# Kernel optimization log

Measured on AMD Instinct MI355X. Metric: run time of the kernel, lower is better.

The kernel has to match this reference:

```python
import jax, jax.numpy as jnp
import numpy as np

SPARSITY = 0.01
NUM_BLOCKS = 8

def _softshrink(v, lam):
    return jnp.sign(v) * jnp.maximum(jnp.abs(v) - lam, 0.0)

def setup_inputs() -> dict:
    key = jax.random.key(0)
    ks = jax.random.split(key, 5)
    B, H, W, C = 4, 128, 128, 768
    nb, bs = NUM_BLOCKS, C // NUM_BLOCKS
    return {
        "x": jax.random.normal(ks[0], (B, H, W, C), dtype=jnp.float32),
        "w1": jax.random.normal(ks[1], (2, nb, bs, bs), dtype=jnp.float32) * 0.02,
        "b1": jax.random.normal(ks[2], (2, nb, bs), dtype=jnp.float32) * 0.02,
        "w2": jax.random.normal(ks[3], (2, nb, bs, bs), dtype=jnp.float32) * 0.02,
        "b2": jax.random.normal(ks[4], (2, nb, bs), dtype=jnp.float32) * 0.02,
    }

def reference(x, w1, b1, w2, b2):
    B, H, W, C = x.shape
    nb = NUM_BLOCKS
    bs = C // nb
    # FFT token mixing (ortho-normalized), real->complex half-spectrum
    xf = jnp.fft.rfft2(x, axes=(1, 2), norm="ortho")  # [B, H, W//2+1, C]
    Hf, Wf = xf.shape[1], xf.shape[2]
    xr = xf.real.reshape(B, Hf, Wf, nb, bs)
    xi = xf.imag.reshape(B, Hf, Wf, nb, bs)
    # kept_modes = H*W//2+1 with hard_thresholding_fraction=1 >= Wf -> all modes kept
    # Block-diagonal complex MLP layer 1 + GELU (exact, matching torch nn.GELU)
    o1r = jax.nn.gelu(
        jnp.einsum("bhwni,nio->bhwno", xr, w1[0])
        - jnp.einsum("bhwni,nio->bhwno", xi, w1[1]) + b1[0],
        approximate=False)
    o1i = jax.nn.gelu(
        jnp.einsum("bhwni,nio->bhwno", xi, w1[0])
        + jnp.einsum("bhwni,nio->bhwno", xr, w1[1]) + b1[1],
        approximate=False)
    # Layer 2 (complex matmul), then softshrink on real/imag parts
    o2r = (jnp.einsum("bhwni,nio->bhwno", o1r, w2[0])
           - jnp.einsum("bhwni,nio->bhwno", o1i, w2[1]) + b2[0])
    o2i = (jnp.einsum("bhwni,nio->bhwno", o1i, w2[0])
           + jnp.einsum("bhwni,nio->bhwno", o1r, w2[1]) + b2[1])
    o2r = _softshrink(o2r, SPARSITY)
    o2i = _softshrink(o2i, SPARSITY)
    xc = (o2r + 1j * o2i).reshape(B, Hf, Wf, C)
    out = jnp.fft.irfft2(xc, s=(H, W), axes=(1, 2), norm="ortho")
    return out
```

## Files before the change

kernel.cpp:

```cpp
#include <hip/hip_runtime.h>
#include <hip/hip_bf16.h>
#include <math.h>

typedef __bf16 bfx8 __attribute__((ext_vector_type(8)));
typedef __bf16 bfx4 __attribute__((ext_vector_type(4)));
typedef float f32x4 __attribute__((ext_vector_type(4)));

__device__ __forceinline__ int bitrev7(int x) {
  return ((x & 1) << 6) | ((x & 2) << 4) | ((x & 4) << 2) | (x & 8)
       | ((x & 16) >> 2) | ((x & 32) >> 4) | ((x & 64) >> 6);
}

__device__ __forceinline__ void bfly(float& ar, float& ai, float& br, float& bi,
                                     float tc, float ts) {
  float dr = ar - br, di = ai - bi;
  ar += br; ai += bi;
  br = dr * tc - di * ts;
  bi = dr * ts + di * tc;
}

__device__ __forceinline__ void build_tw(float2* tw, float sign, int tid) {
  if (tid < 64) {
    float s_, c_;
    __sincosf(sign * (float)(2.0 * M_PI / 128.0) * (float)tid, &s_, &c_);
    tw[tid] = make_float2(c_, s_);
  }
}

__device__ __forceinline__ void fft_stages04(float (&xr)[4][8], float (&xi)[4][8],
                                             const float2* tw, int wq) {
  #pragma unroll
  for (int a = 0; a < 8; ++a) {
    #pragma unroll
    for (int b = 0; b < 2; ++b) {
      float2 t = tw[wq + 4 * a + 32 * b];
      bfly(xr[b][a], xi[b][a], xr[b + 2][a], xi[b + 2][a], t.x, t.y);
    }
  }
  #pragma unroll
  for (int a = 0; a < 8; ++a) {
    float2 t = tw[2 * (wq + 4 * a)];
    bfly(xr[0][a], xi[0][a], xr[1][a], xi[1][a], t.x, t.y);
    bfly(xr[2][a], xi[2][a], xr[3][a], xi[3][a], t.x, t.y);
  }
  #pragma unroll
  for (int a = 0; a < 4; ++a) {
    float2 t = tw[4 * (wq + 4 * a)];
    #pragma unroll
    for (int b = 0; b < 4; ++b)
      bfly(xr[b][a], xi[b][a], xr[b][a + 4], xi[b][a + 4], t.x, t.y);
  }
  {
    float2 t0 = tw[8 * wq];
    float2 t1 = tw[8 * (wq + 4)];
    #pragma unroll
    for (int b = 0; b < 4; ++b) {
      bfly(xr[b][0], xi[b][0], xr[b][2], xi[b][2], t0.x, t0.y);
      bfly(xr[b][1], xi[b][1], xr[b][3], xi[b][3], t1.x, t1.y);
      bfly(xr[b][4], xi[b][4], xr[b][6], xi[b][6], t0.x, t0.y);
      bfly(xr[b][5], xi[b][5], xr[b][7], xi[b][7], t1.x, t1.y);
    }
  }
  {
    float2 t = tw[16 * wq];
    #pragma unroll
    for (int b = 0; b < 4; ++b) {
      #pragma unroll
      for (int a = 0; a < 8; a += 2)
        bfly(xr[b][a], xi[b][a], xr[b][a + 1], xi[b][a + 1], t.x, t.y);
    }
  }
}

__device__ __forceinline__ void fft_stages56(float (&yr)[4], float (&yi)[4], float sign) {
  float dr, di;
  dr = yr[0] - yr[2]; di = yi[0] - yi[2];
  yr[0] += yr[2]; yi[0] += yi[2]; yr[2] = dr; yi[2] = di;
  dr = yr[1] - yr[3]; di = yi[1] - yi[3];
  yr[1] += yr[3]; yi[1] += yi[3];
  yr[3] = -sign * di; yi[3] = sign * dr;
  dr = yr[0] - yr[1]; di = yi[0] - yi[1];
  yr[0] += yr[1]; yi[0] += yi[1]; yr[1] = dr; yi[1] = di;
  dr = yr[2] - yr[3]; di = yi[2] - yi[3];
  yr[2] += yr[3]; yi[2] += yi[3]; yr[3] = dr; yi[3] = di;
}

__global__ __launch_bounds__(256, 2) void k_fftw_fwd(
    const float* __restrict__ x, float* __restrict__ Xr, float* __restrict__ Xi) {
  __shared__ float2 l[128 * 64];
  __shared__ float2 tw[64];
  const int bh = blockIdx.x;
  const int c0 = blockIdx.y * 64;
  const int tid = threadIdx.x;
  const int c = tid & 63, wq = tid >> 6;
  build_tw(tw, -1.f, tid);
  const float* xrow = x + (size_t)bh * (128 * 768) + c0 + c;
  float xr[4][8], xi_[4][8];
  #pragma unroll
  for (int b = 0; b < 4; ++b)
    #pragma unroll
    for (int a = 0; a < 8; ++a) {
      int p = wq + 4 * a + 32 * b;
      xr[b][a] = xrow[(size_t)p * 768];
      xi_[b][a] = 0.f;
    }
  __syncthreads();
  fft_stages04(xr, xi_, tw, wq);
  #pragma unroll
  for (int b = 0; b < 4; ++b)
    #pragma unroll
    for (int a = 0; a < 8; ++a) {
      int p = wq + 4 * a + 32 * b;
      l[p * 64 + c] = make_float2(xr[b][a], xi_[b][a]);
    }
  __syncthreads();
  const float sc = 1.f / 128.f;
  #pragma unroll
  for (int t = 0; t < 8; ++t) {
    int g = wq + 4 * t;
    float yr[4], yi[4];
    #pragma unroll
    for (int d = 0; d < 4; ++d) {
      float2 v = l[(4 * g + d) * 64 + c];
      yr[d] = v.x; yi[d] = v.y;
    }
    fft_stages56(yr, yi, -1.f);
    #pragma unroll
    for (int d = 0; d < 4; ++d) {
      int f = bitrev7(4 * g + d);
      if (f < 65) {
        Xr[((size_t)bh * 65 + f) * 768 + c0 + c]  = yr[d] * sc;
        Xi[((size_t)bh * 128 + f) * 768 + c0 + c] = yi[d] * sc;
      }
    }
  }
}

__global__ __launch_bounds__(256, 2) void k_ffth(
    float* Xr, float* Xi, float sign, float scale) {
  __shared__ float2 l[128 * 64];
  __shared__ float2 tw[64];
  const int bw = blockIdx.x;
  const int b = bw / 65, wf = bw % 65;
  const int c0 = blockIdx.y * 64;
  const int tid = threadIdx.x;
  const int c = tid & 63, wq = tid >> 6;
  build_tw(tw, sign, tid);
  const size_t baser = ((size_t)b * 128 * 65 + wf) * 768 + c0 + c;
  const size_t basei = ((size_t)b * 128 * 128 + wf) * 768 + c0 + c;
  float xr[4][8], xi_[4][8];
  #pragma unroll
  for (int bb = 0; bb < 4; ++bb)
    #pragma unroll
    for (int a = 0; a < 8; ++a) {
      int p = wq + 4 * a + 32 * bb;
      xr[bb][a]  = Xr[baser + (size_t)p * (65 * 768)];
      xi_[bb][a] = Xi[basei + (size_t)p * (128 * 768)];
    }
  __syncthreads();
  fft_stages04(xr, xi_, tw, wq);
  #pragma unroll
  for (int bb = 0; bb < 4; ++bb)
    #pragma unroll
    for (int a = 0; a < 8; ++a) {
      int p = wq + 4 * a + 32 * bb;
      l[p * 64 + c] = make_float2(xr[bb][a], xi_[bb][a]);
    }
  __syncthreads();
  #pragma unroll
  for (int t = 0; t < 8; ++t) {
    int g = wq + 4 * t;
    float yr[4], yi[4];
    #pragma unroll
    for (int d = 0; d < 4; ++d) {
      float2 v = l[(4 * g + d) * 64 + c];
      yr[d] = v.x; yi[d] = v.y;
    }
    fft_stages56(yr, yi, sign);
    #pragma unroll
    for (int d = 0; d < 4; ++d) {
      int hf = bitrev7(4 * g + d);
      Xr[baser + (size_t)hf * (65 * 768)]  = yr[d] * scale;
      Xi[basei + (size_t)hf * (128 * 768)] = yi[d] * scale;
    }
  }
}

__global__ void k_wprep(const float* __restrict__ w1, const float* __restrict__ w2,
                        float* __restrict__ out) {
  int e = blockIdx.x * 256 + threadIdx.x;
  int kin8 = e % 12;
  int t = e / 12;
  int oc = t % 96;
  int t2 = t / 96;
  int n = t2 & 7;
  int q = t2 >> 3;
  int L = q >> 1, ri = q & 1;
  const float* src = (L ? w2 : w1) + (size_t)ri * 73728 + ((size_t)n * 96) * 96 + oc;
  bfx8 v;
  #pragma unroll
  for (int j = 0; j < 8; ++j)
    v[j] = (__bf16)src[(size_t)(kin8 * 8 + j) * 96];
  __bf16* wt = (__bf16*)(out + ((size_t)q * 128 + 65) * 768);
  *(bfx8*)&wt[((size_t)(n * 96 + oc)) * 96 + kin8 * 8] = v;
}

#define MPB 208
__device__ __forceinline__ bfx8 neg8(bfx8 v) {
  union { bfx8 b; unsigned int u[4]; } t;
  t.b = v;
  t.u[0] ^= 0x80008000u; t.u[1] ^= 0x80008000u;
  t.u[2] ^= 0x80008000u; t.u[3] ^= 0x80008000u;
  return t.b;
}

__global__ __launch_bounds__(256, 4) void k_mlp(
    float* __restrict__ Xr, float* __restrict__ Xi,
    const __bf16* __restrict__ wt0,
    const float* __restrict__ b1, const float* __restrict__ b2) {
  __shared__ __align__(16) unsigned char O1[2 * 64 * MPB];

  const int n = blockIdx.y;
  const int m0 = blockIdx.x * 64;
  const int tid = threadIdx.x;
  const int lane = tid & 63;
  const int w = tid >> 6;
  const int col = lane & 15;
  const int quad = lane >> 4;
  const int mrow = w * 16 + col;
  const int m = m0 + mrow;
  const int bh = m / 65, wf = m - bh * 65;
  const size_t xr_base = (size_t)m * 768 + n * 96;
  const size_t xi_base = ((size_t)bh * 128 + wf) * 768 + n * 96;
  const __bf16* w1r = wt0 + (size_t)n * 9216;
  const __bf16* w1i = w1r + 196608;
  const __bf16* w2r = w1r + 2 * 196608;
  const __bf16* w2i = w1r + 3 * 196608;

  const f32x4 fz = { 0.f, 0.f, 0.f, 0.f };
  f32x4 accR[6], accI[6];
  #pragma unroll
  for (int ct = 0; ct < 6; ++ct) { accR[ct] = fz; accI[ct] = fz; }

  #pragma unroll
  for (int kc = 0; kc < 3; ++kc) {
    const int kb = kc * 32 + quad * 8;
    float4 vr0 = *(const float4*)&Xr[xr_base + kb];
    float4 vr1 = *(const float4*)&Xr[xr_base + kb + 4];
    float4 vi0 = *(const float4*)&Xi[xi_base + kb];
    float4 vi1 = *(const float4*)&Xi[xi_base + kb + 4];
    bfx8 axr = { (__bf16)vr0.x, (__bf16)vr0.y, (__bf16)vr0.z, (__bf16)vr0.w,
                 (__bf16)vr1.x, (__bf16)vr1.y, (__bf16)vr1.z, (__bf16)vr1.w };
    bfx8 axi = { (__bf16)vi0.x, (__bf16)vi0.y, (__bf16)vi0.z, (__bf16)vi0.w,
                 (__bf16)vi1.x, (__bf16)vi1.y, (__bf16)vi1.z, (__bf16)vi1.w };
    bfx8 axin = neg8(axi);
    #pragma unroll
    for (int ct = 0; ct < 6; ++ct) {
      const size_t wb = (size_t)(ct * 16 + col) * 96 + kb;
      bfx8 bwr = *(const bfx8*)&w1r[wb];
      bfx8 bwi = *(const bfx8*)&w1i[wb];
      accR[ct] = __builtin_amdgcn_mfma_f32_16x16x32_bf16(axr,  bwr, accR[ct], 0, 0, 0);
      accR[ct] = __builtin_amdgcn_mfma_f32_16x16x32_bf16(axin, bwi, accR[ct], 0, 0, 0);
      accI[ct] = __builtin_amdgcn_mfma_f32_16x16x32_bf16(axi,  bwr, accI[ct], 0, 0, 0);
      accI[ct] = __builtin_amdgcn_mfma_f32_16x16x32_bf16(axr,  bwi, accI[ct], 0, 0, 0);
    }
  }

  #pragma unroll
  for (int ct = 0; ct < 6; ++ct) {
    int oc = ct * 16 + col;
    float br = b1[n * 96 + oc];
    float bi = b1[768 + n * 96 + oc];
    #pragma unroll
    for (int r = 0; r < 4; ++r) {
      int row = w * 16 + quad * 4 + r;
      float vr = accR[ct][r] + br;
      float vi = accI[ct][r] + bi;
      vr = 0.5f * vr * (1.f + erff(vr * 0.70710678118654752f));
      vi = 0.5f * vi * (1.f + erff(vi * 0.70710678118654752f));
      int mask = ((row >> 2) & 3) << 4;
      *(__bf16*)&O1[row * MPB + ((oc * 2) ^ mask)]             = (__bf16)vr;
      *(__bf16*)&O1[64 * MPB + row * MPB + ((oc * 2) ^ mask)]  = (__bf16)vi;
    }
  }
  asm volatile("s_waitcnt lgkmcnt(0)" ::: "memory");

  #pragma unroll
  for (int ct = 0; ct < 6; ++ct) { accR[ct] = fz; accI[ct] = fz; }
  const int amask = ((mrow >> 2) & 3) << 4;
  #pragma unroll
  for (int kc = 0; kc < 3; ++kc) {
    const int kb = kc * 32 + quad * 8;
    const int bc = (kb * 2) ^ amask;
    bfx8 axr = *(const bfx8*)&O1[mrow * MPB + bc];
    bfx8 axi = *(const bfx8*)&O1[64 * MPB + mrow * MPB + bc];
    bfx8 axin = neg8(axi);
    #pragma unroll
    for (int ct = 0; ct < 6; ++ct) {
      const size_t wb = (size_t)(ct * 16 + col) * 96 + kb;
      bfx8 bwr = *(const bfx8*)&w2r[wb];
      bfx8 bwi = *(const bfx8*)&w2i[wb];
      accR[ct] = __builtin_amdgcn_mfma_f32_16x16x32_bf16(axr,  bwr, accR[ct], 0, 0, 0);
      accR[ct] = __builtin_amdgcn_mfma_f32_16x16x32_bf16(axin, bwi, accR[ct], 0, 0, 0);
      accI[ct] = __builtin_amdgcn_mfma_f32_16x16x32_bf16(axi,  bwr, accI[ct], 0, 0, 0);
      accI[ct] = __builtin_amdgcn_mfma_f32_16x16x32_bf16(axr,  bwi, accI[ct], 0, 0, 0);
    }
  }

  #pragma unroll
  for (int ct = 0; ct < 6; ++ct) {
    int oc = ct * 16 + col;
    float br = b2[n * 96 + oc];
    float bi = b2[768 + n * 96 + oc];
    #pragma unroll
    for (int r = 0; r < 4; ++r) {
      int mm = m0 + w * 16 + quad * 4 + r;
      int bh2 = mm / 65, wf2 = mm - bh2 * 65;
      float vr = accR[ct][r] + br;
      float vi = accI[ct][r] + bi;
      vr = (vr > 0.01f) ? vr - 0.01f : ((vr < -0.01f) ? vr + 0.01f : 0.f);
      vi = (vi > 0.01f) ? vi - 0.01f : ((vi < -0.01f) ? vi + 0.01f : 0.f);
      Xr[(size_t)mm * 768 + n * 96 + oc] = vr;
      Xi[((size_t)bh2 * 128 + wf2) * 768 + n * 96 + oc] = vi;
    }
  }
}

__global__ __launch_bounds__(256, 2) void k_ifftw(
    const float* __restrict__ Xr, float* io) {
  __shared__ float2 l[128 * 64];
  __shared__ float2 tw[64];
  const int bh = blockIdx.x;
  const int c0 = blockIdx.y * 64;
  const int tid = threadIdx.x;
  const int c = tid & 63, wq = tid >> 6;
  build_tw(tw, +1.f, tid);
  float xr[4][8], xi_[4][8];
  #pragma unroll
  for (int b = 0; b < 4; ++b)
    #pragma unroll
    for (int a = 0; a < 8; ++a) {
      int p = wq + 4 * a + 32 * b;
      int src = (p <= 64) ? p : 128 - p;
      float sg = (p <= 64) ? 1.f : -1.f;
      xr[b][a]  = Xr[((size_t)bh * 65 + src) * 768 + c0 + c];
      xi_[b][a] = sg * io[((size_t)bh * 128 + src) * 768 + c0 + c];
    }
  __syncthreads();
  fft_stages04(xr, xi_, tw, wq);
  #pragma unroll
  for (int b = 0; b < 4; ++b)
    #pragma unroll
    for (int a = 0; a < 8; ++a) {
      int p = wq + 4 * a + 32 * b;
      l[p * 64 + c] = make_float2(xr[b][a], xi_[b][a]);
    }
  __syncthreads();
  #pragma unroll
  for (int t = 0; t < 8; ++t) {
    int g = wq + 4 * t;
    float yr[4], yi[4];
    #pragma unroll
    for (int d = 0; d < 4; ++d) {
      float2 v = l[(4 * g + d) * 64 + c];
      yr[d] = v.x; yi[d] = v.y;
    }
    fft_stages56(yr, yi, +1.f);
    #pragma unroll
    for (int d = 0; d < 4; ++d) {
      int w = bitrev7(4 * g + d);
      io[((size_t)bh * 128 + w) * 768 + c0 + c] = yr[d];
    }
  }
}

extern "C" void kernel_launch(void* const* d_in, const int* in_sizes, int n_in,
                              void* d_out, int out_size, void* d_ws, size_t ws_size,
                              hipStream_t stream) {
  const float* x  = (const float*)d_in[0];
  const float* w1 = (const float*)d_in[1];
  const float* b1 = (const float*)d_in[2];
  const float* w2 = (const float*)d_in[3];
  const float* b2 = (const float*)d_in[4];
  float* out = (float*)d_out;
  float* Xr = (float*)d_ws;
  float* Xi = out;
  const __bf16* wt0 = (const __bf16*)(out + (size_t)65 * 768);

  dim3 blk(256);
  k_wprep  <<<dim3(144),      blk, 0, stream>>>(w1, w2, out);
  k_fftw_fwd<<<dim3(512, 12), blk, 0, stream>>>(x, Xr, Xi);
  k_ffth   <<<dim3(260, 12),  blk, 0, stream>>>(Xr, Xi, -1.f, 1.f);
  k_mlp    <<<dim3(520, 8),   blk, 0, stream>>>(Xr, Xi, wt0, b1, b2);
  k_ffth   <<<dim3(260, 12),  blk, 0, stream>>>(Xr, Xi, +1.f, 1.f / 128.f);
  k_ifftw  <<<dim3(512, 12),  blk, 0, stream>>>(Xr, out);
}
```

Baseline: 750.4 us.

## Replace LDS transpose for final FFT stages with intra-wavefront shuffles

The final two radix-2 FFT stages in the forward-W, H-axis and inverse-W kernels now run with cross-lane xor shuffles instead of a 64KB shared-memory transpose. The thread-to-data mapping changes so that each wavefront holds 16 channels and all four wq groups, which lets the stage-5/6 partners be exchanged within a wave. This removes the large LDS buffer, a barrier and the LDS round trip, which should also raise occupancy. In exchange it adds shuffle instructions, and each global access now covers 16 contiguous channels per row group instead of 64, which may reduce memory coalescing.

```diff
diff --git a/kernel.cpp b/kernel.cpp
--- a/kernel.cpp
+++ b/kernel.cpp
@@ -72,29 +72,42 @@
   }
 }
 
-__device__ __forceinline__ void fft_stages56(float (&yr)[4], float (&yi)[4], float sign) {
-  float dr, di;
-  dr = yr[0] - yr[2]; di = yi[0] - yi[2];
-  yr[0] += yr[2]; yi[0] += yi[2]; yr[2] = dr; yi[2] = di;
-  dr = yr[1] - yr[3]; di = yi[1] - yi[3];
-  yr[1] += yr[3]; yi[1] += yi[3];
-  yr[3] = -sign * di; yi[3] = sign * dr;
-  dr = yr[0] - yr[1]; di = yi[0] - yi[1];
-  yr[0] += yr[1]; yi[0] += yi[1]; yr[1] = dr; yi[1] = di;
-  dr = yr[2] - yr[3]; di = yi[2] - yi[3];
-  yr[2] += yr[3]; yi[2] += yi[3]; yr[3] = dr; yi[3] = di;
+__device__ __forceinline__ void fft_stages56_shfl(float (&xr)[4][8], float (&xi)[4][8],
+                                                  float sign, int lane) {
+  const bool lo5 = (lane & 32) != 0;
+  const bool odd = (lane & 16) != 0;
+  #pragma unroll
+  for (int b = 0; b < 4; ++b)
+    #pragma unroll
+    for (int a = 0; a < 8; ++a) {
+      float vr = xr[b][a], vi = xi[b][a];
+      float pr = __shfl_xor(vr, 32);
+      float pi = __shfl_xor(vi, 32);
+      float sr, si;
+      if (!lo5) { sr = vr + pr; si = vi + pi; }
+      else {
+        float dr = pr - vr, di = pi - vi;
+        if (!odd) { sr = dr;          si = di; }
+        else      { sr = -sign * di;  si = sign * dr; }
+      }
+      float qr = __shfl_xor(sr, 16);
+      float qi = __shfl_xor(si, 16);
+      if (!odd) { xr[b][a] = sr + qr; xi[b][a] = si + qi; }
+      else      { xr[b][a] = qr - sr; xi[b][a] = qi - si; }
+    }
 }
 
 __global__ __launch_bounds__(256, 2) void k_fftw_fwd(
     const float* __restrict__ x, float* __restrict__ Xr, float* __restrict__ Xi) {
-  __shared__ float2 l[128 * 64];
   __shared__ float2 tw[64];
   const int bh = blockIdx.x;
   const int c0 = blockIdx.y * 64;
   const int tid = threadIdx.x;
-  const int c = tid & 63, wq = tid >> 6;
+  const int lane = tid & 63;
+  const int wq = (lane >> 4) & 3;
+  const int c = c0 + ((tid >> 6) << 4) + (lane & 15);
   build_tw(tw, -1.f, tid);
-  const float* xrow = x + (size_t)bh * (128 * 768) + c0 + c;
+  const float* xrow = x + (size_t)bh * (128 * 768) + c;
   float xr[4][8], xi_[4][8];
   #pragma unroll
   for (int b = 0; b < 4; ++b)
@@ -106,48 +119,34 @@
     }
   __syncthreads();
   fft_stages04(xr, xi_, tw, wq);
+  fft_stages56_shfl(xr, xi_, -1.f, lane);
+  const float sc = 1.f / 128.f;
   #pragma unroll
   for (int b = 0; b < 4; ++b)
     #pragma unroll
     for (int a = 0; a < 8; ++a) {
       int p = wq + 4 * a + 32 * b;
-      l[p * 64 + c] = make_float2(xr[b][a], xi_[b][a]);
-    }
-  __syncthreads();
-  const float sc = 1.f / 128.f;
-  #pragma unroll
-  for (int t = 0; t < 8; ++t) {
-    int g = wq + 4 * t;
-    float yr[4], yi[4];
-    #pragma unroll
-    for (int d = 0; d < 4; ++d) {
-      float2 v = l[(4 * g + d) * 64 + c];
-      yr[d] = v.x; yi[d] = v.y;
-    }
-    fft_stages56(yr, yi, -1.f);
-    #pragma unroll
-    for (int d = 0; d < 4; ++d) {
-      int f = bitrev7(4 * g + d);
+      int f = bitrev7(p);
       if (f < 65) {
-        Xr[((size_t)bh * 65 + f) * 768 + c0 + c]  = yr[d] * sc;
-        Xi[((size_t)bh * 128 + f) * 768 + c0 + c] = yi[d] * sc;
+        Xr[((size_t)bh * 65 + f) * 768 + c]  = xr[b][a] * sc;
+        Xi[((size_t)bh * 128 + f) * 768 + c] = xi_[b][a] * sc;
       }
     }
-  }
 }
 
 __global__ __launch_bounds__(256, 2) void k_ffth(
     float* Xr, float* Xi, float sign, float scale) {
-  __shared__ float2 l[128 * 64];
   __shared__ float2 tw[64];
   const int bw = blockIdx.x;
   const int b = bw / 65, wf = bw % 65;
   const int c0 = blockIdx.y * 64;
   const int tid = threadIdx.x;
-  const int c = tid & 63, wq = tid >> 6;
+  const int lane = tid & 63;
+  const int wq = (lane >> 4) & 3;
+  const int c = c0 + ((tid >> 6) << 4) + (lane & 15);
   build_tw(tw, sign, tid);
-  const size_t baser = ((size_t)b * 128 * 65 + wf) * 768 + c0 + c;
-  const size_t basei = ((size_t)b * 128 * 128 + wf) * 768 + c0 + c;
+  const size_t baser = ((size_t)b * 128 * 65 + wf) * 768 + c;
+  const size_t basei = ((size_t)b * 128 * 128 + wf) * 768 + c;
   float xr[4][8], xi_[4][8];
   #pragma unroll
   for (int bb = 0; bb < 4; ++bb)
@@ -159,31 +158,16 @@
     }
   __syncthreads();
   fft_stages04(xr, xi_, tw, wq);
+  fft_stages56_shfl(xr, xi_, sign, lane);
   #pragma unroll
   for (int bb = 0; bb < 4; ++bb)
     #pragma unroll
     for (int a = 0; a < 8; ++a) {
       int p = wq + 4 * a + 32 * bb;
-      l[p * 64 + c] = make_float2(xr[bb][a], xi_[bb][a]);
-    }
-  __syncthreads();
-  #pragma unroll
-  for (int t = 0; t < 8; ++t) {
-    int g = wq + 4 * t;
-    float yr[4], yi[4];
-    #pragma unroll
-    for (int d = 0; d < 4; ++d) {
-      float2 v = l[(4 * g + d) * 64 + c];
-      yr[d] = v.x; yi[d] = v.y;
-    }
-    fft_stages56(yr, yi, sign);
-    #pragma unroll
-    for (int d = 0; d < 4; ++d) {
-      int hf = bitrev7(4 * g + d);
-      Xr[baser + (size_t)hf * (65 * 768)]  = yr[d] * scale;
-      Xi[basei + (size_t)hf * (128 * 768)] = yi[d] * scale;
-    }
-  }
+      int hf = bitrev7(p);
+      Xr[baser + (size_t)hf * (65 * 768)]  = xr[bb][a] * scale;
+      Xi[basei + (size_t)hf * (128 * 768)] = xi_[bb][a] * scale;
+    }
 }
 
 __global__ void k_wprep(const float* __restrict__ w1, const float* __restrict__ w2,
@@ -328,12 +312,13 @@
 
 __global__ __launch_bounds__(256, 2) void k_ifftw(
     const float* __restrict__ Xr, float* io) {
-  __shared__ float2 l[128 * 64];
   __shared__ float2 tw[64];
   const int bh = blockIdx.x;
   const int c0 = blockIdx.y * 64;
   const int tid = threadIdx.x;
-  const int c = tid & 63, wq = tid >> 6;
+  const int lane = tid & 63;
+  const int wq = (lane >> 4) & 3;
+  const int c = c0 + ((tid >> 6) << 4) + (lane & 15);
   build_tw(tw, +1.f, tid);
   float xr[4][8], xi_[4][8];
   #pragma unroll
@@ -343,35 +328,20 @@
       int p = wq + 4 * a + 32 * b;
       int src = (p <= 64) ? p : 128 - p;
       float sg = (p <= 64) ? 1.f : -1.f;
-      xr[b][a]  = Xr[((size_t)bh * 65 + src) * 768 + c0 + c];
-      xi_[b][a] = sg * io[((size_t)bh * 128 + src) * 768 + c0 + c];
+      xr[b][a]  = Xr[((size_t)bh * 65 + src) * 768 + c];
+      xi_[b][a] = sg * io[((size_t)bh * 128 + src) * 768 + c];
     }
   __syncthreads();
   fft_stages04(xr, xi_, tw, wq);
+  fft_stages56_shfl(xr, xi_, +1.f, lane);
   #pragma unroll
   for (int b = 0; b < 4; ++b)
     #pragma unroll
     for (int a = 0; a < 8; ++a) {
       int p = wq + 4 * a + 32 * b;
-      l[p * 64 + c] = make_float2(xr[b][a], xi_[b][a]);
-    }
-  __syncthreads();
-  #pragma unroll
-  for (int t = 0; t < 8; ++t) {
-    int g = wq + 4 * t;
-    float yr[4], yi[4];
-    #pragma unroll
-    for (int d = 0; d < 4; ++d) {
-      float2 v = l[(4 * g + d) * 64 + c];
-      yr[d] = v.x; yi[d] = v.y;
-    }
-    fft_stages56(yr, yi, +1.f);
-    #pragma unroll
-    for (int d = 0; d < 4; ++d) {
-      int w = bitrev7(4 * g + d);
-      io[((size_t)bh * 128 + w) * 768 + c0 + c] = yr[d];
-    }
-  }
+      int w = bitrev7(p);
+      io[((size_t)bh * 128 + w) * 768 + c] = xr[b][a];
+    }
 }
 
 extern "C" void kernel_launch(void* const* d_in, const int* in_sizes, int n_in,
```

Result: slower. 780.9 us (+4.1%).
